# Optimization experiments

Hardware: AMD Instinct MI355X
Metric: run time of the kernel (lower is better)

The kernel has to match this reference:

```python
import jax, jax.numpy as jnp
import numpy as np

N, BSZ, NE, DIN, DH, RH = 32, 512, 7, 512, 256, 64
NPAIR = NE * (NE - 1) // 2  # 21
PAIRS = [(i, j) for i in range(NE) for j in range(i + 1, NE)]


def setup_inputs() -> dict:
    key = jax.random.key(0)
    ks = jax.random.split(key, 16)
    def w(k, shape, fan_in):
        return jax.random.normal(k, shape, jnp.float32) / np.sqrt(fan_in)
    return {
        "input": jax.random.normal(ks[0], (N, BSZ, NE, DIN), jnp.float32),
        "ctx_differences": jax.random.normal(ks[1], (BSZ, NPAIR, 5), jnp.float32),
        "lang_input": jax.random.normal(ks[2], (N, BSZ, 128), jnp.float32),
        "num_markables": jax.random.randint(ks[3], (BSZ,), 0, N),
        # unary feedforward: 2 hidden layers + output layer (output_dim=2)
        "W0": w(ks[4], (DIN, DH), DIN), "b0": jnp.zeros((DH,), jnp.float32),
        "W1": w(ks[5], (DH, DH), DH), "b1": jnp.zeros((DH,), jnp.float32),
        "W2": w(ks[6], (DH, 2), DH), "b2": jnp.zeros((2,), jnp.float32),
        # relation encoder: 1 hidden layer (dim 64), output 3
        "R0": w(ks[7], (5, RH), 5), "r0": jnp.zeros((RH,), jnp.float32),
        "R1": w(ks[8], (RH, 3), RH), "r1": jnp.zeros((3,), jnp.float32),
    }


def reference(input, ctx_differences, lang_input, num_markables,
              W0, b0, W1, b1, W2, b2, R0, r0, R1, r1):
    # unary potentials: [N, bsz, 7, 2]
    h = jax.nn.relu(input @ W0 + b0)
    h = jax.nn.relu(h @ W1 + b1)
    un = h @ W2 + b2
    # binary potentials: [bsz, 21, 3] -> map to 2x2 via fixed matrix
    h2 = jax.nn.relu(ctx_differences @ R0 + r0)
    bp3 = h2 @ R1 + r1
    Mmap = jnp.array([[1, 0, 0], [0, 1, 0], [0, 1, 0], [0, 0, 1]], jnp.float32)
    bp4 = jnp.einsum('bpx,yx->bpy', bp3, Mmap).reshape(BSZ, NPAIR, 2, 2)

    # accumulate log-factors into the joint log tensor [N, bsz, 2,...,2]
    joint = jnp.zeros((N, BSZ) + (2,) * NE, jnp.float32)
    for i in range(NE):
        shp = [N, BSZ] + [1] * NE
        shp[2 + i] = 2
        joint = joint + un[:, :, i].reshape(shp)
    for p, (i, j) in enumerate(PAIRS):
        shp = [1, BSZ] + [1] * NE
        shp[2 + i] = 2
        shp[2 + j] = 2
        joint = joint + bp4[:, p].reshape(shp)

    # marginals: logsumexp over all entity axes but one -> [N, bsz, 7, 2]
    ent_axes = tuple(range(2, 2 + NE))
    marg = jnp.stack(
        [jax.scipy.special.logsumexp(joint, axis=tuple(a for a in ent_axes if a != 2 + i))
         for i in range(NE)], axis=2)
    lm = jax.nn.log_softmax(marg, axis=-1)
    marginal_log_probs = lm[..., 1] - lm[..., 0]  # [N, bsz, 7]

    jf = joint.reshape(N, BSZ, 2 ** NE)
    joint_log_probs = jax.nn.log_softmax(jf, axis=-1).reshape((N, BSZ) + (2,) * NE)
    return (marginal_log_probs, joint_log_probs)
```

## Files before the change

### kernel.cpp

```cpp
#include <hip/hip_runtime.h>

typedef __bf16 bf16;
typedef bf16 bf16x8 __attribute__((ext_vector_type(8)));
typedef bf16 bf16x4 __attribute__((ext_vector_type(4)));
typedef float f32x4 __attribute__((ext_vector_type(4)));

#define MFMA(a, b, c) __builtin_amdgcn_mfma_f32_16x16x32_bf16((a), (b), (c), 0, 0, 0)


__global__ __launch_bounds__(256) void k_prep(const float* __restrict__ W0,
                                              const float* __restrict__ W1,
                                              const float* __restrict__ W2,
                                              bf16* __restrict__ W0f,
                                              bf16* __restrict__ W1f,
                                              bf16* __restrict__ W2f) {
  int g = blockIdx.x * 256 + threadIdx.x;
  if (g < 16384) {
    int mt = g >> 10, ks = (g >> 6) & 15, lane = g & 63;
    int m = mt * 16 + (lane & 15);
    int kb = ks * 32 + (lane >> 4) * 8;
    bf16x8 v;
#pragma unroll
    for (int j = 0; j < 8; ++j) v[j] = (bf16)W0[(kb + j) * 256 + m];
    *(bf16x8*)&W0f[g * 8] = v;
  } else if (g < 24576) {
    int h = g - 16384;
    int mt = h >> 9, ks = (h >> 6) & 7, lane = h & 63;
    int m = mt * 16 + (lane & 15);
    int kb = ks * 32 + (lane >> 4) * 8;
    bf16x8 v;
#pragma unroll
    for (int j = 0; j < 8; ++j) v[j] = (bf16)W1[(kb + j) * 256 + m];
    *(bf16x8*)&W1f[h * 8] = v;
  } else {
    int h = g - 24576;
    int ks = h >> 6, lane = h & 63;
    int c = lane & 15;
    int kb = ks * 32 + (lane >> 4) * 8;
    bf16x8 v;
#pragma unroll
    for (int j = 0; j < 8; ++j) v[j] = (c < 2) ? (bf16)W2[(kb + j) * 2 + c] : (bf16)0.0f;
    *(bf16x8*)&W2f[h * 8] = v;
  }
}

__global__ __launch_bounds__(256, 3) void k_unary(const float* __restrict__ input,
                                                  const bf16* __restrict__ W0f,
                                                  const bf16* __restrict__ W1f,
                                                  const bf16* __restrict__ W2f,
                                                  const float* __restrict__ b0,
                                                  const float* __restrict__ b1,
                                                  const float* __restrict__ b2,
                                                  float* __restrict__ un) {
  __shared__ bf16 inp_lds[2][64 * 72];
  __shared__ bf16 h_lds[64 * 264];

  const int tid = threadIdx.x;
  const int wave = tid >> 6;
  const int lane = tid & 63;
  const int l16 = lane & 15;
  const int lq = lane >> 4;
  const long m0 = (long)blockIdx.x * 64;

  f32x4 acc[4][4];
#pragma unroll
  for (int i = 0; i < 4; ++i)
#pragma unroll
    for (int j = 0; j < 4; ++j) acc[i][j] = (f32x4){0.f, 0.f, 0.f, 0.f};

  const int r = tid >> 2;
  const int q = tid & 3;
  const float* gp = input + (m0 + r) * 512 + q * 16;
  float4 x0 = *(const float4*)(gp + 0);
  float4 x1 = *(const float4*)(gp + 4);
  float4 x2 = *(const float4*)(gp + 8);
  float4 x3 = *(const float4*)(gp + 12);

#define STAGE(BUF)                                                              \
  do {                                                                          \
    bf16x8 wlo, whi;                                                            \
    wlo[0] = (bf16)x0.x; wlo[1] = (bf16)x0.y; wlo[2] = (bf16)x0.z;              \
    wlo[3] = (bf16)x0.w; wlo[4] = (bf16)x1.x; wlo[5] = (bf16)x1.y;              \
    wlo[6] = (bf16)x1.z; wlo[7] = (bf16)x1.w;                                   \
    whi[0] = (bf16)x2.x; whi[1] = (bf16)x2.y; whi[2] = (bf16)x2.z;              \
    whi[3] = (bf16)x2.w; whi[4] = (bf16)x3.x; whi[5] = (bf16)x3.y;              \
    whi[6] = (bf16)x3.z; whi[7] = (bf16)x3.w;                                   \
    *(bf16x8*)&inp_lds[BUF][r * 72 + q * 16] = wlo;                             \
    *(bf16x8*)&inp_lds[BUF][r * 72 + q * 16 + 8] = whi;                         \
  } while (0)

  STAGE(0);
  __syncthreads();

  for (int it = 0; it < 8; ++it) {
    const int cur = it & 1;
    if (it < 7) {
      gp += 64;
      x0 = *(const float4*)(gp + 0);
      x1 = *(const float4*)(gp + 4);
      x2 = *(const float4*)(gp + 8);
      x3 = *(const float4*)(gp + 12);
    }
    bf16x8 afr[2][4];
#pragma unroll
    for (int kk = 0; kk < 2; ++kk)
#pragma unroll
      for (int mt = 0; mt < 4; ++mt)
        afr[kk][mt] =
            *(const bf16x8*)&W0f[(((wave * 4 + mt) * 16 + it * 2 + kk) * 64 + lane) * 8];
#pragma unroll
    for (int kk = 0; kk < 2; ++kk) {
      bf16x8 bfr[4];
#pragma unroll
      for (int nt = 0; nt < 4; ++nt)
        bfr[nt] = *(const bf16x8*)&inp_lds[cur][(nt * 16 + l16) * 72 + kk * 32 + lq * 8];
#pragma unroll
      for (int mt = 0; mt < 4; ++mt)
#pragma unroll
        for (int nt = 0; nt < 4; ++nt) acc[mt][nt] = MFMA(afr[kk][mt], bfr[nt], acc[mt][nt]);
    }
    if (it < 7) STAGE(cur ^ 1);
    __syncthreads();
  }
#undef STAGE

#pragma unroll
  for (int mt = 0; mt < 4; ++mt) {
    const int nbase = (wave * 4 + mt) * 16 + lq * 4;
    const float4 bb = *(const float4*)&b0[nbase];
#pragma unroll
    for (int nt = 0; nt < 4; ++nt) {
      const int m = nt * 16 + l16;
      bf16x4 hv;
      hv[0] = (bf16)fmaxf(acc[mt][nt][0] + bb.x, 0.f);
      hv[1] = (bf16)fmaxf(acc[mt][nt][1] + bb.y, 0.f);
      hv[2] = (bf16)fmaxf(acc[mt][nt][2] + bb.z, 0.f);
      hv[3] = (bf16)fmaxf(acc[mt][nt][3] + bb.w, 0.f);
      *(bf16x4*)&h_lds[m * 264 + nbase] = hv;
    }
  }
  __syncthreads();

#pragma unroll
  for (int i = 0; i < 4; ++i)
#pragma unroll
    for (int j = 0; j < 4; ++j) acc[i][j] = (f32x4){0.f, 0.f, 0.f, 0.f};
  for (int ks = 0; ks < 8; ++ks) {
    bf16x8 bfr[4];
#pragma unroll
    for (int nt = 0; nt < 4; ++nt)
      bfr[nt] = *(const bf16x8*)&h_lds[(nt * 16 + l16) * 264 + ks * 32 + lq * 8];
#pragma unroll
    for (int mt = 0; mt < 4; ++mt) {
      bf16x8 a = *(const bf16x8*)&W1f[(((wave * 4 + mt) * 8 + ks) * 64 + lane) * 8];
#pragma unroll
      for (int nt = 0; nt < 4; ++nt) acc[mt][nt] = MFMA(a, bfr[nt], acc[mt][nt]);
    }
  }
  __syncthreads();

#pragma unroll
  for (int mt = 0; mt < 4; ++mt) {
    const int nbase = (wave * 4 + mt) * 16 + lq * 4;
    const float4 bb = *(const float4*)&b1[nbase];
#pragma unroll
    for (int nt = 0; nt < 4; ++nt) {
      const int m = nt * 16 + l16;
      bf16x4 hv;
      hv[0] = (bf16)fmaxf(acc[mt][nt][0] + bb.x, 0.f);
      hv[1] = (bf16)fmaxf(acc[mt][nt][1] + bb.y, 0.f);
      hv[2] = (bf16)fmaxf(acc[mt][nt][2] + bb.z, 0.f);
      hv[3] = (bf16)fmaxf(acc[mt][nt][3] + bb.w, 0.f);
      *(bf16x4*)&h_lds[m * 264 + nbase] = hv;
    }
  }
  __syncthreads();

  float* part = (float*)&inp_lds[0][0];
  f32x4 acc2[4];
#pragma unroll
  for (int i = 0; i < 4; ++i) acc2[i] = (f32x4){0.f, 0.f, 0.f, 0.f};
#pragma unroll
  for (int s = 0; s < 2; ++s) {
    const int ks = wave * 2 + s;
    bf16x8 a = *(const bf16x8*)&W2f[(ks * 64 + lane) * 8];
#pragma unroll
    for (int nt = 0; nt < 4; ++nt) {
      bf16x8 b = *(const bf16x8*)&h_lds[(nt * 16 + l16) * 264 + ks * 32 + lq * 8];
      acc2[nt] = MFMA(a, b, acc2[nt]);
    }
  }
  if (lane < 16) {
#pragma unroll
    for (int nt = 0; nt < 4; ++nt) {
      part[((wave * 4 + nt) * 16 + lane) * 2 + 0] = acc2[nt][0];
      part[((wave * 4 + nt) * 16 + lane) * 2 + 1] = acc2[nt][1];
    }
  }
  __syncthreads();
  if (tid < 128) {
    const int mloc = tid >> 1, c = tid & 1;
    const int nt = mloc >> 4, l = mloc & 15;
    float s = b2[c];
#pragma unroll
    for (int w2 = 0; w2 < 4; ++w2) s += part[((w2 * 4 + nt) * 16 + l) * 2 + c];
    un[(m0 + mloc) * 2 + c] = s;
  }
}

__global__ __launch_bounds__(128) void k_bsum(const float* __restrict__ ctx,
                                              const float* __restrict__ R0,
                                              const float* __restrict__ r0,
                                              const float* __restrict__ R1,
                                              const float* __restrict__ r1,
                                              float* __restrict__ bsum) {
  __shared__ float ctx_l[105], R0_l[320], r0_l[64], R1_l[192], r1_l[3];
  __shared__ float h2[21 * 65];
  __shared__ float bp[63];
  const int t = threadIdx.x;
  const int b = blockIdx.x;
  if (t < 105) ctx_l[t] = ctx[b * 105 + t];
  for (int i = t; i < 320; i += 128) R0_l[i] = R0[i];
  if (t < 64) r0_l[t] = r0[t];
  for (int i = t; i < 192; i += 128) R1_l[i] = R1[i];
  if (t < 3) r1_l[t] = r1[t];
  __syncthreads();
  for (int idx = t; idx < 1344; idx += 128) {
    int p = idx >> 6, u = idx & 63;
    float a = r0_l[u];
#pragma unroll
    for (int x = 0; x < 5; ++x) a += ctx_l[p * 5 + x] * R0_l[x * 64 + u];
    h2[p * 65 + u] = fmaxf(a, 0.f);
  }
  __syncthreads();
  if (t < 63) {
    int p = t / 3, y = t - p * 3;
    float a = r1_l[y];
    for (int u = 0; u < 64; ++u) a += h2[p * 65 + u] * R1_l[u * 3 + y];
    bp[t] = a;
  }
  __syncthreads();
  float a = 0.f;
  int pi = 0;
#pragma unroll
  for (int i = 0; i < 7; ++i)
#pragma unroll
    for (int j = i + 1; j < 7; ++j) {
      int bi = (t >> (6 - i)) & 1, bj = (t >> (6 - j)) & 1;
      a += bp[pi * 3 + bi + bj];
      ++pi;
    }
  bsum[b * 128 + t] = a;
}

__global__ __launch_bounds__(256) void k_joint(const float* __restrict__ un,
                                               const float* __restrict__ bsum,
                                               float* __restrict__ out_marg,
                                               float* __restrict__ out_joint) {
  const int lane = threadIdx.x & 63;
  const int w = threadIdx.x >> 6;
  const int wrow = __builtin_amdgcn_readfirstlane(blockIdx.x * 4 + w);
  const int b = wrow & 511;

  const float* up = un + (long)wrow * 14;
  float u[14];
#pragma unroll
  for (int k = 0; k < 14; ++k) u[k] = up[k];

  const float* bp = bsum + b * 128;
  const float bs_lo = bp[lane];
  const float bs_hi = bp[64 + lane];

  float umid = 0.f;
#pragma unroll
  for (int i = 1; i < 7; ++i) umid += u[2 * i + ((lane >> (6 - i)) & 1)];
  const float j_lo = bs_lo + umid + u[0];
  const float j_hi = bs_hi + umid + u[1];

  float mm = fmaxf(j_lo, j_hi);
#pragma unroll
  for (int o = 32; o; o >>= 1) mm = fmaxf(mm, __shfl_xor(mm, o, 64));
  const float e_lo = __expf(j_lo - mm);
  const float e_hi = __expf(j_hi - mm);
  const float c = e_lo + e_hi;

  float a1 = c + __shfl_xor(c, 16, 64);
  float A  = a1 + __shfl_xor(a1, 32, 64);
  float e1 = c + __shfl_xor(c, 4, 64);
  float E23 = e1 + __shfl_xor(e1, 8, 64);
  float r1_ = A + __shfl_xor(A, 4, 64);
  float R2345 = r1_ + __shfl_xor(r1_, 8, 64);
  float s1_ = A + __shfl_xor(A, 1, 64);
  float R0145 = s1_ + __shfl_xor(s1_, 2, 64);
  float u1_ = E23 + __shfl_xor(E23, 1, 64);
  float R0123 = u1_ + __shfl_xor(u1_, 2, 64);

  float v0 = R2345 + __shfl_xor(R2345, 2, 64);
  float v1 = R2345 + __shfl_xor(R2345, 1, 64);
  float v2 = R0145 + __shfl_xor(R0145, 8, 64);
  float v3 = R0145 + __shfl_xor(R0145, 4, 64);
  float v4 = R0123 + __shfl_xor(R0123, 32, 64);
  float v5 = R0123 + __shfl_xor(R0123, 16, 64);
  const float T = v0 + __shfl_xor(v0, 1, 64);

  float th = e_hi;
#pragma unroll
  for (int o = 32; o; o >>= 1) th += __shfl_xor(th, o, 64);

  const float lT = __logf(T);
  float* oj = out_joint + (long)wrow * 128;
  oj[lane] = (j_lo - mm) - lT;
  oj[64 + lane] = (j_hi - mm) - lT;

  const float S0 = __shfl(v0, 1, 64);
  const float S1 = __shfl(v1, 2, 64);
  const float S2 = __shfl(v2, 4, 64);
  const float S3 = __shfl(v3, 8, 64);
  const float S4 = __shfl(v4, 16, 64);
  const float S5 = __shfl(v5, 32, 64);
  if (lane < 7) {
    const float s1v = (lane == 0) ? th
                    : (lane == 1) ? S5
                    : (lane == 2) ? S4
                    : (lane == 3) ? S3
                    : (lane == 4) ? S2
                    : (lane == 5) ? S1 : S0;
    const float s0v = T - s1v;
    out_marg[(long)wrow * 7 + lane] = __logf(s1v) - __logf(s0v);
  }
}

extern "C" void kernel_launch(void* const* d_in, const int* in_sizes, int n_in,
                              void* d_out, int out_size, void* d_ws, size_t ws_size,
                              hipStream_t stream) {
  const float* input = (const float*)d_in[0];
  const float* ctx   = (const float*)d_in[1];
  const float* W0 = (const float*)d_in[4];
  const float* b0 = (const float*)d_in[5];
  const float* W1 = (const float*)d_in[6];
  const float* b1 = (const float*)d_in[7];
  const float* W2 = (const float*)d_in[8];
  const float* b2 = (const float*)d_in[9];
  const float* R0 = (const float*)d_in[10];
  const float* r0 = (const float*)d_in[11];
  const float* R1 = (const float*)d_in[12];
  const float* r1 = (const float*)d_in[13];

  char* ws = (char*)d_ws;
  bf16* W0f  = (bf16*)(ws + 0);
  bf16* W1f  = (bf16*)(ws + 262144);
  bf16* W2f  = (bf16*)(ws + 393216);
  float* un  = (float*)(ws + 401408);
  float* bsm = (float*)(ws + 1318912);

  float* out_marg = (float*)d_out;
  float* out_joint = out_marg + 114688;

  hipLaunchKernelGGL(k_prep, dim3(98), dim3(256), 0, stream, W0, W1, W2, W0f, W1f, W2f);
  hipLaunchKernelGGL(k_bsum, dim3(512), dim3(128), 0, stream, ctx, R0, r0, R1, r1, bsm);
  hipLaunchKernelGGL(k_unary, dim3(1792), dim3(256), 0, stream,
                     input, W0f, W1f, W2f, b0, b1, b2, un);
  hipLaunchKernelGGL(k_joint, dim3(4096), dim3(256), 0, stream, un, bsm, out_marg, out_joint);
}
```

Before: 381.7 us.

## Load layer-0 input fragments directly from global; merge prep and bsum kernels

Layer 0 of the unary MLP no longer stages the fp32 input through double-buffered LDS with block barriers. Each lane now loads its MFMA B fragment straight from global memory, converts it to bf16 in registers, and walks K in 16 steps of 32. Separately, the weight-prep and pairwise-bsum kernels are merged into one launch to save a kernel launch. This removes LDS traffic and syncs from the main loop and frees LDS for occupancy. In exchange, global loads become less coalesced (16-row strided float4 reads) and are no longer overlapped with compute through explicit prefetch.

```diff
diff --git a/kernel.cpp b/kernel.cpp
--- a/kernel.cpp
+++ b/kernel.cpp
@@ -8,39 +8,87 @@
 #define MFMA(a, b, c) __builtin_amdgcn_mfma_f32_16x16x32_bf16((a), (b), (c), 0, 0, 0)
 
 
-__global__ __launch_bounds__(256) void k_prep(const float* __restrict__ W0,
-                                              const float* __restrict__ W1,
-                                              const float* __restrict__ W2,
-                                              bf16* __restrict__ W0f,
-                                              bf16* __restrict__ W1f,
-                                              bf16* __restrict__ W2f) {
-  int g = blockIdx.x * 256 + threadIdx.x;
-  if (g < 16384) {
-    int mt = g >> 10, ks = (g >> 6) & 15, lane = g & 63;
-    int m = mt * 16 + (lane & 15);
-    int kb = ks * 32 + (lane >> 4) * 8;
-    bf16x8 v;
-#pragma unroll
-    for (int j = 0; j < 8; ++j) v[j] = (bf16)W0[(kb + j) * 256 + m];
-    *(bf16x8*)&W0f[g * 8] = v;
-  } else if (g < 24576) {
-    int h = g - 16384;
-    int mt = h >> 9, ks = (h >> 6) & 7, lane = h & 63;
-    int m = mt * 16 + (lane & 15);
-    int kb = ks * 32 + (lane >> 4) * 8;
-    bf16x8 v;
-#pragma unroll
-    for (int j = 0; j < 8; ++j) v[j] = (bf16)W1[(kb + j) * 256 + m];
-    *(bf16x8*)&W1f[h * 8] = v;
-  } else {
-    int h = g - 24576;
-    int ks = h >> 6, lane = h & 63;
-    int c = lane & 15;
-    int kb = ks * 32 + (lane >> 4) * 8;
-    bf16x8 v;
-#pragma unroll
-    for (int j = 0; j < 8; ++j) v[j] = (c < 2) ? (bf16)W2[(kb + j) * 2 + c] : (bf16)0.0f;
-    *(bf16x8*)&W2f[h * 8] = v;
+__global__ __launch_bounds__(256) void k_small(const float* __restrict__ ctx,
+                                               const float* __restrict__ R0,
+                                               const float* __restrict__ r0,
+                                               const float* __restrict__ R1,
+                                               const float* __restrict__ r1,
+                                               float* __restrict__ bsum,
+                                               const float* __restrict__ W0,
+                                               const float* __restrict__ W1,
+                                               const float* __restrict__ W2,
+                                               bf16* __restrict__ W0f,
+                                               bf16* __restrict__ W1f,
+                                               bf16* __restrict__ W2f) {
+  const int t = threadIdx.x;
+  if (blockIdx.x >= 512) {
+    int g = (blockIdx.x - 512) * 256 + t;
+    if (g < 16384) {
+      int mt = g >> 10, ks = (g >> 6) & 15, lane = g & 63;
+      int m = mt * 16 + (lane & 15);
+      int kb = ks * 32 + (lane >> 4) * 8;
+      bf16x8 v;
+#pragma unroll
+      for (int j = 0; j < 8; ++j) v[j] = (bf16)W0[(kb + j) * 256 + m];
+      *(bf16x8*)&W0f[g * 8] = v;
+    } else if (g < 24576) {
+      int h = g - 16384;
+      int mt = h >> 9, ks = (h >> 6) & 7, lane = h & 63;
+      int m = mt * 16 + (lane & 15);
+      int kb = ks * 32 + (lane >> 4) * 8;
+      bf16x8 v;
+#pragma unroll
+      for (int j = 0; j < 8; ++j) v[j] = (bf16)W1[(kb + j) * 256 + m];
+      *(bf16x8*)&W1f[h * 8] = v;
+    } else {
+      int h = g - 24576;
+      int ks = h >> 6, lane = h & 63;
+      int c = lane & 15;
+      int kb = ks * 32 + (lane >> 4) * 8;
+      bf16x8 v;
+#pragma unroll
+      for (int j = 0; j < 8; ++j) v[j] = (c < 2) ? (bf16)W2[(kb + j) * 2 + c] : (bf16)0.0f;
+      *(bf16x8*)&W2f[h * 8] = v;
+    }
+    return;
+  }
+  __shared__ float ctx_l[105], R0_l[320], r0_l[64], R1_l[192], r1_l[3];
+  __shared__ float h2[21 * 65];
+  __shared__ float bp[63];
+  const int b = blockIdx.x;
+  if (t < 105) ctx_l[t] = ctx[b * 105 + t];
+  for (int i = t; i < 320; i += 256) R0_l[i] = R0[i];
+  if (t < 64) r0_l[t] = r0[t];
+  if (t < 192) R1_l[t] = R1[t];
+  if (t < 3) r1_l[t] = r1[t];
+  __syncthreads();
+  for (int idx = t; idx < 1344; idx += 256) {
+    int p = idx >> 6, u = idx & 63;
+    float a = r0_l[u];
+#pragma unroll
+    for (int x = 0; x < 5; ++x) a += ctx_l[p * 5 + x] * R0_l[x * 64 + u];
+    h2[p * 65 + u] = fmaxf(a, 0.f);
+  }
+  __syncthreads();
+  if (t < 63) {
+    int p = t / 3, y = t - p * 3;
+    float a = r1_l[y];
+    for (int u = 0; u < 64; ++u) a += h2[p * 65 + u] * R1_l[u * 3 + y];
+    bp[t] = a;
+  }
+  __syncthreads();
+  if (t < 128) {
+    float a = 0.f;
+    int pi = 0;
+#pragma unroll
+    for (int i = 0; i < 7; ++i)
+#pragma unroll
+      for (int j = i + 1; j < 7; ++j) {
+        int bi = (t >> (6 - i)) & 1, bj = (t >> (6 - j)) & 1;
+        a += bp[pi * 3 + bi + bj];
+        ++pi;
+      }
+    bsum[b * 128 + t] = a;
   }
 }
 
@@ -52,8 +100,8 @@
                                                   const float* __restrict__ b1,
                                                   const float* __restrict__ b2,
                                                   float* __restrict__ un) {
-  __shared__ bf16 inp_lds[2][64 * 72];
   __shared__ bf16 h_lds[64 * 264];
+  __shared__ float part_lds[512];
 
   const int tid = threadIdx.x;
   const int wave = tid >> 6;
@@ -68,61 +116,27 @@
 #pragma unroll
     for (int j = 0; j < 4; ++j) acc[i][j] = (f32x4){0.f, 0.f, 0.f, 0.f};
 
-  const int r = tid >> 2;
-  const int q = tid & 3;
-  const float* gp = input + (m0 + r) * 512 + q * 16;
-  float4 x0 = *(const float4*)(gp + 0);
-  float4 x1 = *(const float4*)(gp + 4);
-  float4 x2 = *(const float4*)(gp + 8);
-  float4 x3 = *(const float4*)(gp + 12);
-
-#define STAGE(BUF)                                                              \
-  do {                                                                          \
-    bf16x8 wlo, whi;                                                            \
-    wlo[0] = (bf16)x0.x; wlo[1] = (bf16)x0.y; wlo[2] = (bf16)x0.z;              \
-    wlo[3] = (bf16)x0.w; wlo[4] = (bf16)x1.x; wlo[5] = (bf16)x1.y;              \
-    wlo[6] = (bf16)x1.z; wlo[7] = (bf16)x1.w;                                   \
-    whi[0] = (bf16)x2.x; whi[1] = (bf16)x2.y; whi[2] = (bf16)x2.z;              \
-    whi[3] = (bf16)x2.w; whi[4] = (bf16)x3.x; whi[5] = (bf16)x3.y;              \
-    whi[6] = (bf16)x3.z; whi[7] = (bf16)x3.w;                                   \
-    *(bf16x8*)&inp_lds[BUF][r * 72 + q * 16] = wlo;                             \
-    *(bf16x8*)&inp_lds[BUF][r * 72 + q * 16 + 8] = whi;                         \
-  } while (0)
-
-  STAGE(0);
-  __syncthreads();
-
-  for (int it = 0; it < 8; ++it) {
-    const int cur = it & 1;
-    if (it < 7) {
-      gp += 64;
-      x0 = *(const float4*)(gp + 0);
-      x1 = *(const float4*)(gp + 4);
-      x2 = *(const float4*)(gp + 8);
-      x3 = *(const float4*)(gp + 12);
-    }
-    bf16x8 afr[2][4];
-#pragma unroll
-    for (int kk = 0; kk < 2; ++kk)
-#pragma unroll
-      for (int mt = 0; mt < 4; ++mt)
-        afr[kk][mt] =
-            *(const bf16x8*)&W0f[(((wave * 4 + mt) * 16 + it * 2 + kk) * 64 + lane) * 8];
-#pragma unroll
-    for (int kk = 0; kk < 2; ++kk) {
-      bf16x8 bfr[4];
-#pragma unroll
-      for (int nt = 0; nt < 4; ++nt)
-        bfr[nt] = *(const bf16x8*)&inp_lds[cur][(nt * 16 + l16) * 72 + kk * 32 + lq * 8];
-#pragma unroll
-      for (int mt = 0; mt < 4; ++mt)
-#pragma unroll
-        for (int nt = 0; nt < 4; ++nt) acc[mt][nt] = MFMA(afr[kk][mt], bfr[nt], acc[mt][nt]);
-    }
-    if (it < 7) STAGE(cur ^ 1);
-    __syncthreads();
-  }
-#undef STAGE
+  const float* bbase = input + (m0 + l16) * 512 + lq * 8;
+#pragma unroll 2
+  for (int it = 0; it < 16; ++it) {
+    bf16x8 bfr[4];
+#pragma unroll
+    for (int nt = 0; nt < 4; ++nt) {
+      const float* p = bbase + nt * (16 * 512) + it * 32;
+      float4 lo = *(const float4*)p;
+      float4 hi = *(const float4*)(p + 4);
+      bf16x8 v;
+      v[0] = (bf16)lo.x; v[1] = (bf16)lo.y; v[2] = (bf16)lo.z; v[3] = (bf16)lo.w;
+      v[4] = (bf16)hi.x; v[5] = (bf16)hi.y; v[6] = (bf16)hi.z; v[7] = (bf16)hi.w;
+      bfr[nt] = v;
+    }
+#pragma unroll
+    for (int mt = 0; mt < 4; ++mt) {
+      bf16x8 a = *(const bf16x8*)&W0f[(((wave * 4 + mt) * 16 + it) * 64 + lane) * 8];
+#pragma unroll
+      for (int nt = 0; nt < 4; ++nt) acc[mt][nt] = MFMA(a, bfr[nt], acc[mt][nt]);
+    }
+  }
 
 #pragma unroll
   for (int mt = 0; mt < 4; ++mt) {
@@ -176,7 +190,6 @@
   }
   __syncthreads();
 
-  float* part = (float*)&inp_lds[0][0];
   f32x4 acc2[4];
 #pragma unroll
   for (int i = 0; i < 4; ++i) acc2[i] = (f32x4){0.f, 0.f, 0.f, 0.f};
@@ -193,8 +206,8 @@
   if (lane < 16) {
 #pragma unroll
     for (int nt = 0; nt < 4; ++nt) {
-      part[((wave * 4 + nt) * 16 + lane) * 2 + 0] = acc2[nt][0];
-      part[((wave * 4 + nt) * 16 + lane) * 2 + 1] = acc2[nt][1];
+      part_lds[((wave * 4 + nt) * 16 + lane) * 2 + 0] = acc2[nt][0];
+      part_lds[((wave * 4 + nt) * 16 + lane) * 2 + 1] = acc2[nt][1];
     }
   }
   __syncthreads();
@@ -203,54 +216,9 @@
     const int nt = mloc >> 4, l = mloc & 15;
     float s = b2[c];
 #pragma unroll
-    for (int w2 = 0; w2 < 4; ++w2) s += part[((w2 * 4 + nt) * 16 + l) * 2 + c];
+    for (int w2 = 0; w2 < 4; ++w2) s += part_lds[((w2 * 4 + nt) * 16 + l) * 2 + c];
     un[(m0 + mloc) * 2 + c] = s;
   }
-}
-
-__global__ __launch_bounds__(128) void k_bsum(const float* __restrict__ ctx,
-                                              const float* __restrict__ R0,
-                                              const float* __restrict__ r0,
-                                              const float* __restrict__ R1,
-                                              const float* __restrict__ r1,
-                                              float* __restrict__ bsum) {
-  __shared__ float ctx_l[105], R0_l[320], r0_l[64], R1_l[192], r1_l[3];
-  __shared__ float h2[21 * 65];
-  __shared__ float bp[63];
-  const int t = threadIdx.x;
-  const int b = blockIdx.x;
-  if (t < 105) ctx_l[t] = ctx[b * 105 + t];
-  for (int i = t; i < 320; i += 128) R0_l[i] = R0[i];
-  if (t < 64) r0_l[t] = r0[t];
-  for (int i = t; i < 192; i += 128) R1_l[i] = R1[i];
-  if (t < 3) r1_l[t] = r1[t];
-  __syncthreads();
-  for (int idx = t; idx < 1344; idx += 128) {
-    int p = idx >> 6, u = idx & 63;
-    float a = r0_l[u];
-#pragma unroll
-    for (int x = 0; x < 5; ++x) a += ctx_l[p * 5 + x] * R0_l[x * 64 + u];
-    h2[p * 65 + u] = fmaxf(a, 0.f);
-  }
-  __syncthreads();
-  if (t < 63) {
-    int p = t / 3, y = t - p * 3;
-    float a = r1_l[y];
-    for (int u = 0; u < 64; ++u) a += h2[p * 65 + u] * R1_l[u * 3 + y];
-    bp[t] = a;
-  }
-  __syncthreads();
-  float a = 0.f;
-  int pi = 0;
-#pragma unroll
-  for (int i = 0; i < 7; ++i)
-#pragma unroll
-    for (int j = i + 1; j < 7; ++j) {
-      int bi = (t >> (6 - i)) & 1, bj = (t >> (6 - j)) & 1;
-      a += bp[pi * 3 + bi + bj];
-      ++pi;
-    }
-  bsum[b * 128 + t] = a;
 }
 
 __global__ __launch_bounds__(256) void k_joint(const float* __restrict__ un,
@@ -356,8 +324,8 @@
   float* out_marg = (float*)d_out;
   float* out_joint = out_marg + 114688;
 
-  hipLaunchKernelGGL(k_prep, dim3(98), dim3(256), 0, stream, W0, W1, W2, W0f, W1f, W2f);
-  hipLaunchKernelGGL(k_bsum, dim3(512), dim3(128), 0, stream, ctx, R0, r0, R1, r1, bsm);
+  hipLaunchKernelGGL(k_small, dim3(610), dim3(256), 0, stream,
+                     ctx, R0, r0, R1, r1, bsm, W0, W1, W2, W0f, W1f, W2f);
   hipLaunchKernelGGL(k_unary, dim3(1792), dim3(256), 0, stream,
                      input, W0f, W1f, W2f, b0, b1, b2, un);
   hipLaunchKernelGGL(k_joint, dim3(4096), dim3(256), 0, stream, un, bsm, out_marg, out_joint);
```

Measured after the change: 464.9 us. +21.8%, slower.
